# Kernel tuning notes

Measured on AMD Instinct MI355X. Metric: run time of the kernel, lower is better.

## Reference

```python
import jax, jax.numpy as jnp
import numpy as np

GRID_SIZE = 5


def kan_layer(x, spline_weight, spline_scaler, grid):
    # x: (B, In); spline_weight: (Out, In, G); spline_scaler: (Out, In); grid: (G,)
    xn = jnp.tanh(x)                                   # (B, In)
    # distances: (B, Out, In, G) via broadcast of (B,1,In,1) against (G,)
    distances = jnp.abs(xn[:, None, :, None] - grid)
    weights = jnp.exp(-distances * spline_scaler[None, :, :, None])
    # double sum over grid then in_features, fused into one einsum
    return jnp.einsum('boig,oig->bo', weights, spline_weight)


def setup_inputs() -> dict:
    key = jax.random.key(0)
    ks = jax.random.split(key, 7)
    B, D_IN, D_H, D_OUT = 2048, 128, 256, 64
    return {
        'x':  jax.random.normal(ks[0], (B, D_IN), dtype=jnp.float32),
        'w1': jax.random.normal(ks[1], (D_H, D_IN, GRID_SIZE), dtype=jnp.float32),
        's1': jax.random.normal(ks[2], (D_H, D_IN), dtype=jnp.float32),
        'w2': jax.random.normal(ks[3], (D_H // 2, D_H, GRID_SIZE), dtype=jnp.float32),
        's2': jax.random.normal(ks[4], (D_H // 2, D_H), dtype=jnp.float32),
        'w3': jax.random.normal(ks[5], (D_OUT, D_H // 2, GRID_SIZE), dtype=jnp.float32),
        's3': jax.random.normal(ks[6], (D_OUT, D_H // 2), dtype=jnp.float32),
    }


def reference(x, w1, s1, w2, s2, w3, s3):
    grid = jnp.linspace(-1.0, 1.0, GRID_SIZE, dtype=jnp.float32)  # registered buffer
    h1 = jax.nn.relu(kan_layer(x, w1, s1, grid))
    h2 = jax.nn.relu(kan_layer(h1, w2, s2, grid))
    out = jax.nn.sigmoid(kan_layer(h2, w3, s3, grid))
    return out
```

## Files before the change

kernel.cpp:

```cpp
#include <hip/hip_runtime.h>
#include <math.h>

#define GRID_N 5
#define LOG2E 1.4426950408889634f
#define EXP2F __builtin_amdgcn_exp2f
#define BATCH 2048

__device__ __forceinline__ void prep_one(const float* __restrict__ w,
                                         const float* __restrict__ s,
                                         float* __restrict__ T, float* __restrict__ Kt,
                                         int O, int I, int idx) {
    int o = idx / I, i = idx % I;
    float K = -s[idx] * LOG2E;
    const float gv[5] = {-1.f, -0.5f, 0.f, 0.5f, 1.f};
    float A[6], B[6];
    A[0] = 0.f; B[5] = 0.f;
#pragma unroll
    for (int g = 0; g < 5; g++)
        A[g + 1] = A[g] + w[idx * GRID_N + g] * EXP2F(-K * gv[g]);
#pragma unroll
    for (int g = 4; g >= 0; g--)
        B[g] = B[g + 1] + w[idx * GRID_N + g] * EXP2F(K * gv[g]);
#pragma unroll
    for (int k = 0; k < 6; k++) {
        T[((i * 6 + k) * O + o) * 2 + 0] = A[k];
        T[((i * 6 + k) * O + o) * 2 + 1] = B[k];
    }
    Kt[i * O + o] = K;
}

__global__ __launch_bounds__(256) void prep_all(
    const float* __restrict__ w1, const float* __restrict__ s1, float* T1, float* K1,
    const float* __restrict__ w2, const float* __restrict__ s2, float* T2, float* K2,
    const float* __restrict__ w3, const float* __restrict__ s3, float* T3, float* K3) {
    int idx = blockIdx.x * 256 + threadIdx.x;
    if (idx < 32768)       prep_one(w1, s1, T1, K1, 256, 128, idx);
    else if (idx < 65536)  prep_one(w2, s2, T2, K2, 128, 256, idx - 32768);
    else if (idx < 73728)  prep_one(w3, s3, T3, K3,  64, 128, idx - 65536);
}

#define LOADB(lb, AB, KV)                                                      \
    _Pragma("unroll")                                                          \
    for (int u = 0; u < 8; u++) {                                              \
        const int l  = (lb) * 8 + u;                                           \
        const int gi = hbase + c * 64 + l;                                     \
        KV[u] = Kt[gi * OUT + o];                                              \
        _Pragma("unroll")                                                      \
        for (int j = 0; j < BPT; j++) {                                        \
            unsigned os = (unsigned)__builtin_amdgcn_readlane((int)off[j][c], l); \
            AB[j][u] = *(const float2*)(Tb + (os + o8));                       \
        }                                                                      \
    }

#define COMPB(lb, AB, KV)                                                      \
    _Pragma("unroll")                                                          \
    for (int u = 0; u < 8; u++) {                                              \
        const int l = (lb) * 8 + u;                                            \
        _Pragma("unroll")                                                      \
        for (int j = 0; j < BPT; j++) {                                        \
            float xs = __int_as_float(__builtin_amdgcn_readlane(__float_as_int(xv[j][c]), l)); \
            float t  = KV[u] * xs;                                             \
            acc[j] += AB[j][u].x * EXP2F(t) + AB[j][u].y * EXP2F(-t);          \
        }                                                                      \
    }

template<int LEN, int OUT, int OCH, int BPT, int HALVES, int EPI, int XMODE>
__global__ __launch_bounds__(256) __attribute__((amdgpu_waves_per_eu(4, 4)))
void kan_pipe(const float* __restrict__ xin,
              const char*  __restrict__ Tb,
              const float* __restrict__ Kt,
              float* __restrict__ outp)
{
    constexpr int CH   = LEN / 64;
    constexpr int NBG  = BATCH / BPT;
    constexpr int XSTR = LEN * HALVES;
    constexpr unsigned ROWB = OUT * 8;

    const int lane = threadIdx.x & 63;
    const int wid  = (blockIdx.x << 2) | (threadIdx.x >> 6);
    const int oc   = wid / (NBG * HALVES);
    const int rem  = wid % (NBG * HALVES);
    const int h    = rem / NBG;
    const int bg   = rem % NBG;
    const int o    = (oc << 6) | lane;
    const int b0   = bg * BPT;
    const int hbase = h * LEN;

    float    xv[BPT][CH];
    unsigned off[BPT][CH];
#pragma unroll
    for (int j = 0; j < BPT; j++)
#pragma unroll
        for (int c = 0; c < CH; c++) {
            const int gi = hbase + (c << 6) + lane;
            float v;
            if (XMODE == 0) {
                v = xin[(b0 + j) * XSTR + gi];
            } else {
                int e = (b0 + j) * XSTR + gi;
                v = fmaxf(xin[e] + xin[BATCH * XSTR + e], 0.f);
            }
            float ex = EXP2F(2.0f * LOG2E * v);
            float t  = 1.0f - 2.0f / (ex + 1.0f);
            xv[j][c] = t;
            int k = (int)((t + 1.0f) * 2.0f) + 1;
            k = k > 5 ? 5 : k;
            off[j][c] = (unsigned)(gi * 6 + k) * ROWB;
        }

    float acc[BPT];
#pragma unroll
    for (int j = 0; j < BPT; j++) acc[j] = 0.f;

    const unsigned o8 = (unsigned)o * 8u;

#pragma unroll
    for (int c = 0; c < CH; c++) {
        float2 abA[BPT][8], abB[BPT][8];
        float  KvA[8], KvB[8];
        LOADB(0, abA, KvA);
#pragma unroll
        for (int p = 0; p < 3; p++) {
            LOADB(2 * p + 1, abB, KvB);
            COMPB(2 * p,     abA, KvA);
            LOADB(2 * p + 2, abA, KvA);
            COMPB(2 * p + 1, abB, KvB);
        }
        LOADB(7, abB, KvB);
        COMPB(6, abA, KvA);
        COMPB(7, abB, KvB);
    }

#pragma unroll
    for (int j = 0; j < BPT; j++) {
        float z = acc[j];
        if (EPI == 0) z = fmaxf(z, 0.f);
        outp[(h * BATCH + (b0 + j)) * OUT + o] = z;
    }
}

__global__ __launch_bounds__(256) void sigmoid_combine(
    const float* __restrict__ p, float* __restrict__ out, int n) {
    int e = blockIdx.x * 256 + threadIdx.x;
    if (e >= n) return;
    float z = p[e] + p[n + e];
    out[e] = 1.0f / (1.0f + EXP2F(-LOG2E * z));
}

extern "C" void kernel_launch(void* const* d_in, const int* in_sizes, int n_in,
                              void* d_out, int out_size, void* d_ws, size_t ws_size,
                              hipStream_t stream) {
    const float* x  = (const float*)d_in[0];
    const float* w1 = (const float*)d_in[1];
    const float* s1 = (const float*)d_in[2];
    const float* w2 = (const float*)d_in[3];
    const float* s2 = (const float*)d_in[4];
    const float* w3 = (const float*)d_in[5];
    const float* s3 = (const float*)d_in[6];
    float* out = (float*)d_out;

    float* ws  = (float*)d_ws;
    float* h1  = ws;
    float* p2  = h1  + 524288;
    float* T1  = p2  + 524288;
    float* K1  = T1  + 393216;
    float* T2  = K1  + 32768;
    float* K2  = T2  + 393216;
    float* T3  = K2  + 32768;
    float* K3  = T3  + 98304;
    float* p3  = h1;

    prep_all<<<288, 256, 0, stream>>>(w1, s1, T1, K1, w2, s2, T2, K2, w3, s3, T3, K3);

    kan_pipe<128, 256, 4, 2, 1, 0, 0><<<1024, 256, 0, stream>>>(
        x, (const char*)T1, K1, h1);
    kan_pipe<128, 128, 2, 2, 2, 1, 0><<<1024, 256, 0, stream>>>(
        h1, (const char*)T2, K2, p2);
    kan_pipe<64, 64, 1, 2, 2, 1, 1><<<512, 256, 0, stream>>>(
        p2, (const char*)T3, K3, p3);
    sigmoid_combine<<<512, 256, 0, stream>>>(p3, out, 131072);
}
```

Measured before the change: 101.1 us.

## Replace software-pipelined KAN kernel with block-synchronized lockstep waves sharing outputs

Drops the explicit double-buffered register prefetch and instead has the four waves of a block cover the same output columns for consecutive batch rows. A __syncthreads at each phase keeps the waves in lockstep so their table and K loads hit cache together. Each wave now handles four batch rows instead of two, which halves the grid. The waves_per_eu hint is removed and p3 gets its own buffer. The cost is barrier stalls and less latency hiding within each wave.

```diff
diff --git a/kernel.cpp b/kernel.cpp
--- a/kernel.cpp
+++ b/kernel.cpp
@@ -39,51 +39,27 @@
     else if (idx < 73728)  prep_one(w3, s3, T3, K3,  64, 128, idx - 65536);
 }
 
-#define LOADB(lb, AB, KV)                                                      \
-    _Pragma("unroll")                                                          \
-    for (int u = 0; u < 8; u++) {                                              \
-        const int l  = (lb) * 8 + u;                                           \
-        const int gi = hbase + c * 64 + l;                                     \
-        KV[u] = Kt[gi * OUT + o];                                              \
-        _Pragma("unroll")                                                      \
-        for (int j = 0; j < BPT; j++) {                                        \
-            unsigned os = (unsigned)__builtin_amdgcn_readlane((int)off[j][c], l); \
-            AB[j][u] = *(const float2*)(Tb + (os + o8));                       \
-        }                                                                      \
-    }
-
-#define COMPB(lb, AB, KV)                                                      \
-    _Pragma("unroll")                                                          \
-    for (int u = 0; u < 8; u++) {                                              \
-        const int l = (lb) * 8 + u;                                            \
-        _Pragma("unroll")                                                      \
-        for (int j = 0; j < BPT; j++) {                                        \
-            float xs = __int_as_float(__builtin_amdgcn_readlane(__float_as_int(xv[j][c]), l)); \
-            float t  = KV[u] * xs;                                             \
-            acc[j] += AB[j][u].x * EXP2F(t) + AB[j][u].y * EXP2F(-t);          \
-        }                                                                      \
-    }
-
 template<int LEN, int OUT, int OCH, int BPT, int HALVES, int EPI, int XMODE>
-__global__ __launch_bounds__(256) __attribute__((amdgpu_waves_per_eu(4, 4)))
-void kan_pipe(const float* __restrict__ xin,
-              const char*  __restrict__ Tb,
-              const float* __restrict__ Kt,
-              float* __restrict__ outp)
+__global__ __launch_bounds__(256) void kan_sync(
+    const float* __restrict__ xin,
+    const char*  __restrict__ Tb,
+    const float* __restrict__ Kt,
+    float* __restrict__ outp)
 {
     constexpr int CH   = LEN / 64;
-    constexpr int NBG  = BATCH / BPT;
+    constexpr int ROWS = 4 * BPT;
     constexpr int XSTR = LEN * HALVES;
     constexpr unsigned ROWB = OUT * 8;
 
-    const int lane = threadIdx.x & 63;
-    const int wid  = (blockIdx.x << 2) | (threadIdx.x >> 6);
-    const int oc   = wid / (NBG * HALVES);
-    const int rem  = wid % (NBG * HALVES);
-    const int h    = rem / NBG;
-    const int bg   = rem % NBG;
+    const int tid  = threadIdx.x;
+    const int lane = tid & 63;
+    const int w    = tid >> 6;
+    const int h    = (HALVES > 1) ? (blockIdx.x % HALVES) : 0;
+    const int q    = blockIdx.x / HALVES;
+    const int oc   = q % OCH;
+    const int bb   = q / OCH;
     const int o    = (oc << 6) | lane;
-    const int b0   = bg * BPT;
+    const int b0   = bb * ROWS + w * BPT;
     const int hbase = h * LEN;
 
     float    xv[BPT][CH];
@@ -116,19 +92,28 @@
 
 #pragma unroll
     for (int c = 0; c < CH; c++) {
-        float2 abA[BPT][8], abB[BPT][8];
-        float  KvA[8], KvB[8];
-        LOADB(0, abA, KvA);
+#pragma unroll 1
+        for (int ph = 0; ph < 8; ph++) {
+            __syncthreads();
 #pragma unroll
-        for (int p = 0; p < 3; p++) {
-            LOADB(2 * p + 1, abB, KvB);
-            COMPB(2 * p,     abA, KvA);
-            LOADB(2 * p + 2, abA, KvA);
-            COMPB(2 * p + 1, abB, KvB);
+            for (int u = 0; u < 8; u++) {
+                const int l  = (ph << 3) + u;
+                const int gi = hbase + (c << 6) + l;
+                float Kv = Kt[gi * OUT + o];
+                float2 ab[BPT];
+#pragma unroll
+                for (int j = 0; j < BPT; j++) {
+                    unsigned os = (unsigned)__builtin_amdgcn_readlane((int)off[j][c], l);
+                    ab[j] = *(const float2*)(Tb + (os + o8));
+                }
+#pragma unroll
+                for (int j = 0; j < BPT; j++) {
+                    float xs = __int_as_float(__builtin_amdgcn_readlane(__float_as_int(xv[j][c]), l));
+                    float t  = Kv * xs;
+                    acc[j] += ab[j].x * EXP2F(t) + ab[j].y * EXP2F(-t);
+                }
+            }
         }
-        LOADB(7, abB, KvB);
-        COMPB(6, abA, KvA);
-        COMPB(7, abB, KvB);
     }
 
 #pragma unroll
@@ -162,21 +147,21 @@
     float* ws  = (float*)d_ws;
     float* h1  = ws;
     float* p2  = h1  + 524288;
-    float* T1  = p2  + 524288;
+    float* p3  = p2  + 524288;
+    float* T1  = p3  + 262144;
     float* K1  = T1  + 393216;
     float* T2  = K1  + 32768;
     float* K2  = T2  + 393216;
     float* T3  = K2  + 32768;
     float* K3  = T3  + 98304;
-    float* p3  = h1;
 
     prep_all<<<288, 256, 0, stream>>>(w1, s1, T1, K1, w2, s2, T2, K2, w3, s3, T3, K3);
 
-    kan_pipe<128, 256, 4, 2, 1, 0, 0><<<1024, 256, 0, stream>>>(
+    kan_sync<128, 256, 4, 4, 1, 0, 0><<<512, 256, 0, stream>>>(
         x, (const char*)T1, K1, h1);
-    kan_pipe<128, 128, 2, 2, 2, 1, 0><<<1024, 256, 0, stream>>>(
+    kan_sync<128, 128, 2, 4, 2, 1, 0><<<512, 256, 0, stream>>>(
         h1, (const char*)T2, K2, p2);
-    kan_pipe<64, 64, 1, 2, 2, 1, 1><<<512, 256, 0, stream>>>(
+    kan_sync<64, 64, 1, 4, 2, 1, 1><<<256, 256, 0, stream>>>(
         p2, (const char*)T3, K3, p3);
     sigmoid_combine<<<512, 256, 0, stream>>>(p3, out, 131072);
 }
```

After: 123.8 us. 22.5% more time.

## Drop split-K in layer 2 and add sched barriers between load/compute stages

Applied to the files above, without the earlier changes.

Layer 2 now reduces over the full 256 inputs in one wave (LEN=256, HALVES=1) and applies relu directly. This removes the partial-sum buffer and the combine-on-read XMODE path in layer 3, at the cost of half as many waves for layer 2. Scheduling barriers are inserted between each LOADB/COMPB stage so the compiler keeps the hand-written software pipeline order. The layer-2 output is sliced in two halves for layer 3 via XSTR. Longer per-wave loops and larger unrolled register use in layer 2 may reduce occupancy or latency hiding.

```diff
diff --git a/kernel.cpp b/kernel.cpp
--- a/kernel.cpp
+++ b/kernel.cpp
@@ -5,6 +5,7 @@
 #define LOG2E 1.4426950408889634f
 #define EXP2F __builtin_amdgcn_exp2f
 #define BATCH 2048
+#define SB()  __builtin_amdgcn_sched_barrier(0)
 
 __device__ __forceinline__ void prep_one(const float* __restrict__ w,
                                          const float* __restrict__ s,
@@ -64,7 +65,7 @@
         }                                                                      \
     }
 
-template<int LEN, int OUT, int OCH, int BPT, int HALVES, int EPI, int XMODE>
+template<int LEN, int OUT, int OCH, int BPT, int HALVES, int EPI>
 __global__ __launch_bounds__(256) __attribute__((amdgpu_waves_per_eu(4, 4)))
 void kan_pipe(const float* __restrict__ xin,
               const char*  __restrict__ Tb,
@@ -93,13 +94,7 @@
 #pragma unroll
         for (int c = 0; c < CH; c++) {
             const int gi = hbase + (c << 6) + lane;
-            float v;
-            if (XMODE == 0) {
-                v = xin[(b0 + j) * XSTR + gi];
-            } else {
-                int e = (b0 + j) * XSTR + gi;
-                v = fmaxf(xin[e] + xin[BATCH * XSTR + e], 0.f);
-            }
+            float v  = xin[(b0 + j) * XSTR + gi];
             float ex = EXP2F(2.0f * LOG2E * v);
             float t  = 1.0f - 2.0f / (ex + 1.0f);
             xv[j][c] = t;
@@ -118,17 +113,17 @@
     for (int c = 0; c < CH; c++) {
         float2 abA[BPT][8], abB[BPT][8];
         float  KvA[8], KvB[8];
-        LOADB(0, abA, KvA);
+        LOADB(0, abA, KvA); SB();
 #pragma unroll
         for (int p = 0; p < 3; p++) {
-            LOADB(2 * p + 1, abB, KvB);
-            COMPB(2 * p,     abA, KvA);
-            LOADB(2 * p + 2, abA, KvA);
-            COMPB(2 * p + 1, abB, KvB);
+            LOADB(2 * p + 1, abB, KvB); SB();
+            COMPB(2 * p,     abA, KvA); SB();
+            LOADB(2 * p + 2, abA, KvA); SB();
+            COMPB(2 * p + 1, abB, KvB); SB();
         }
-        LOADB(7, abB, KvB);
-        COMPB(6, abA, KvA);
-        COMPB(7, abB, KvB);
+        LOADB(7, abB, KvB); SB();
+        COMPB(6, abA, KvA); SB();
+        COMPB(7, abB, KvB); SB();
     }
 
 #pragma unroll
@@ -161,22 +156,22 @@
 
     float* ws  = (float*)d_ws;
     float* h1  = ws;
-    float* p2  = h1  + 524288;
-    float* T1  = p2  + 524288;
+    float* h2  = h1  + 524288;
+    float* p3  = h2  + 262144;
+    float* T1  = p3  + 262144;
     float* K1  = T1  + 393216;
     float* T2  = K1  + 32768;
     float* K2  = T2  + 393216;
     float* T3  = K2  + 32768;
     float* K3  = T3  + 98304;
-    float* p3  = h1;
 
     prep_all<<<288, 256, 0, stream>>>(w1, s1, T1, K1, w2, s2, T2, K2, w3, s3, T3, K3);
 
-    kan_pipe<128, 256, 4, 2, 1, 0, 0><<<1024, 256, 0, stream>>>(
+    kan_pipe<128, 256, 4, 2, 1, 0><<<1024, 256, 0, stream>>>(
         x, (const char*)T1, K1, h1);
-    kan_pipe<128, 128, 2, 2, 2, 1, 0><<<1024, 256, 0, stream>>>(
-        h1, (const char*)T2, K2, p2);
-    kan_pipe<64, 64, 1, 2, 2, 1, 1><<<512, 256, 0, stream>>>(
-        p2, (const char*)T3, K3, p3);
+    kan_pipe<256, 128, 2, 2, 1, 0><<<512, 256, 0, stream>>>(
+        h1, (const char*)T2, K2, h2);
+    kan_pipe<64, 64, 1, 2, 2, 1><<<512, 256, 0, stream>>>(
+        h2, (const char*)T3, K3, p3);
     sigmoid_combine<<<512, 256, 0, stream>>>(p3, out, 131072);
 }
```

After: 103.3 us. 1.02x slower.
